# Kernel tuning notes

Hardware: AMD Instinct MI355X
Metric: run time of the kernel (lower is better)

## Reference

```python
import jax, jax.numpy as jnp
import numpy as np

DIM = 1024
N_HEADS = 16
HEAD_DIM = DIM // N_HEADS
MAX_CTX = 2048


def build_rope_cache(seq_len, head_dim, base=10000.0):
    inv_freq = 1.0 / (base ** (jnp.arange(0, head_dim, 2, dtype=jnp.float32) / head_dim))
    t = jnp.arange(seq_len, dtype=jnp.float32)
    freqs = jnp.einsum('i,j->ij', t, inv_freq)  # [T, head_dim//2]
    return jnp.cos(freqs), jnp.sin(freqs)


def apply_rope(x, cos, sin):
    # x: [B, H, T, D]; interleaved even/odd rotation
    x1 = x[..., 0::2]
    x2 = x[..., 1::2]
    c = cos[None, None, :x.shape[-2], :]
    s = sin[None, None, :x.shape[-2], :]
    rx1 = x1 * c - x2 * s
    rx2 = x1 * s + x2 * c
    return jnp.stack([rx1, rx2], axis=-1).reshape(x.shape)


def setup_inputs() -> dict:
    key = jax.random.key(0)
    k1, k2, k3 = jax.random.split(key, 3)
    B, T = 2, 2048
    x = jax.random.normal(k1, (B, T, DIM), dtype=jnp.float32)
    # torch nn.Linear weight shapes: [out_features, in_features]
    qkv_w = jax.random.normal(k2, (3 * DIM, DIM), dtype=jnp.float32) * (1.0 / np.sqrt(DIM))
    out_w = jax.random.normal(k3, (DIM, DIM), dtype=jnp.float32) * (1.0 / np.sqrt(DIM))
    return {"x": x, "qkv_w": qkv_w, "out_w": out_w}


def reference(x, qkv_w, out_w):
    B, T, C = x.shape
    cos, sin = build_rope_cache(MAX_CTX, HEAD_DIM)
    cos = cos.astype(x.dtype)
    sin = sin.astype(x.dtype)

    qkv = jnp.einsum('btc,dc->btd', x, qkv_w)  # [B, T, 3C]
    qkv = qkv.reshape(B, T, 3, N_HEADS, HEAD_DIM).transpose(2, 0, 3, 1, 4)
    q, k, v = qkv[0], qkv[1], qkv[2]  # each [B, H, T, D]

    q = apply_rope(q, cos, sin)
    k = apply_rope(k, cos, sin)

    scale = 1.0 / np.sqrt(HEAD_DIM)
    scores = jnp.einsum('bhqd,bhkd->bhqk', q, k) * scale  # [B, H, T, T]
    causal = jnp.tril(jnp.ones((T, T), dtype=bool))
    scores = jnp.where(causal[None, None], scores, jnp.finfo(scores.dtype).min)
    attn = jax.nn.softmax(scores, axis=-1)
    y = jnp.einsum('bhqk,bhkd->bhqd', attn, v)  # [B, H, T, D]
    y = y.transpose(0, 2, 1, 3).reshape(B, T, C)
    return jnp.einsum('btc,dc->btd', y, out_w)
```

## Files before the change

### kernel.cpp

```cpp
#include <hip/hip_runtime.h>
#include <hip/hip_bf16.h>
#include <cstdint>
#include <cstddef>

#define B_SZ   2
#define T_CTX  2048
#define DIM_C  1024
#define NHEAD  16
#define HD     64
#define NBH    (B_SZ*NHEAD)

typedef __attribute__((ext_vector_type(8))) short short8;
typedef __attribute__((ext_vector_type(4))) float f32x4;
typedef __attribute__((ext_vector_type(16))) float f32x16;

union BV8 { short8 s; __hip_bfloat16 h[8]; unsigned short u[8]; };
union U32x4 { uint32_t u[4]; short8 s8; };

#define GLD16(gp, lp) \
  __builtin_amdgcn_global_load_lds((const __attribute__((address_space(1))) void*)(gp), \
                                   (__attribute__((address_space(3))) void*)(lp), 16, 0, 0)

__device__ inline uint32_t pkbf(float a, float b) {
  union { __hip_bfloat16 h; unsigned short u; } ua, ub;
  ua.h = __float2bfloat16(a);
  ub.h = __float2bfloat16(b);
  return ((uint32_t)ub.u << 16) | (uint32_t)ua.u;
}

__global__ __launch_bounds__(256) void cvt_all(const float* __restrict__ x,
                                               const float* __restrict__ wq,
                                               const float* __restrict__ wo,
                                               __hip_bfloat16* __restrict__ xb,
                                               __hip_bfloat16* __restrict__ wqb,
                                               __hip_bfloat16* __restrict__ wob) {
  int i = blockIdx.x * 256 + threadIdx.x;
  const float* src;
  __hip_bfloat16* dst;
  int off;
  if (i < 1048576) { src = x; dst = xb; off = i; }
  else if (i < 1835008) { src = wq; dst = wqb; off = i - 1048576; }
  else { src = wo; dst = wob; off = i - 1835008; }
  float4 v = reinterpret_cast<const float4*>(src)[off];
  BV8 o;
  o.h[0] = __float2bfloat16(v.x);
  o.h[1] = __float2bfloat16(v.y);
  o.h[2] = __float2bfloat16(v.z);
  o.h[3] = __float2bfloat16(v.w);
  ushort4 st = { o.u[0], o.u[1], o.u[2], o.u[3] };
  reinterpret_cast<ushort4*>(dst)[off] = st;
}

template <typename OutT, int BN>
__global__ __launch_bounds__(256) void gemm_bt(const __hip_bfloat16* __restrict__ A,
                                               const __hip_bfloat16* __restrict__ Bt,
                                               OutT* __restrict__ C,
                                               int M, int N, int K) {
  constexpr int NB = BN / 32;
  constexpr int ABYT = 128 * 128;
  constexpr int BBYT = BN * 128;
  __shared__ __align__(16) char smem[2 * (ABYT + BBYT)];
  const int tid = threadIdx.x;
  const int w = tid >> 6, l = tid & 63;
  const int l15 = l & 15, l4 = l >> 4;
  const int wr = w >> 1, wc = w & 1;
  const int gx = (int)gridDim.x;
  const int nwg = gx * (int)gridDim.y;
  int lin = (int)blockIdx.y * gx + (int)blockIdx.x;
  lin = (lin & 7) * (nwg >> 3) + (lin >> 3);
  const long bm = (long)(lin / gx) * 128;
  const long bn = (long)(lin % gx) * BN;

  f32x4 acc[4][NB] = {};

  const int srow = tid >> 3;
  const int scol = (tid & 7) * 16;
  const int ssw  = scol ^ ((srow & 7) << 4);
  const char* Ab  = (const char*)A;
  const char* Btb = (const char*)Bt;

#define GSTAGE(kt_, buf_)                                                                \
  {                                                                                      \
    char* base_ = smem + (buf_) * (ABYT + BBYT);                                         \
    _Pragma("unroll")                                                                    \
    for (int it = 0; it < 4; ++it) {                                                     \
      long arow = bm + it * 32 + srow;                                                   \
      GLD16(Ab + (arow * K + (kt_)) * 2 + ssw, base_ + it * 4096 + w * 1024);            \
    }                                                                                    \
    _Pragma("unroll")                                                                    \
    for (int it = 0; it < BN / 32; ++it) {                                               \
      long brow = bn + it * 32 + srow;                                                   \
      GLD16(Btb + (brow * K + (kt_)) * 2 + ssw, base_ + ABYT + it * 4096 + w * 1024);    \
    }                                                                                    \
  }

  GSTAGE(0, 0)

  int cur = 0;
  for (int kt = 0; kt < K; kt += 64) {
    __syncthreads();
    if (kt + 64 < K) GSTAGE(kt + 64, cur ^ 1)
    const char* Ac = smem + cur * (ABYT + BBYT);
    const char* Bc = Ac + ABYT;
#pragma unroll
    for (int ksub = 0; ksub < 2; ++ksub) {
      short8 aF[4], bF[NB];
#pragma unroll
      for (int m = 0; m < 4; ++m) {
        int R = wr * 64 + m * 16 + l15;
        aF[m] = *(const short8*)(Ac + R * 128 + ((ksub * 64 + l4 * 16) ^ ((R & 7) << 4)));
      }
#pragma unroll
      for (int n = 0; n < NB; ++n) {
        int R = wc * (BN / 2) + n * 16 + l15;
        bF[n] = *(const short8*)(Bc + R * 128 + ((ksub * 64 + l4 * 16) ^ ((R & 7) << 4)));
      }
#pragma unroll
      for (int m = 0; m < 4; ++m)
#pragma unroll
        for (int n = 0; n < NB; ++n)
          acc[m][n] = __builtin_amdgcn_mfma_f32_16x16x32_bf16(aF[m], bF[n], acc[m][n], 0, 0, 0);
    }
    cur ^= 1;
  }
#undef GSTAGE

#pragma unroll
  for (int m = 0; m < 4; ++m)
#pragma unroll
    for (int n = 0; n < NB; ++n)
#pragma unroll
      for (int r = 0; r < 4; ++r) {
        long row = bm + wr * 64 + m * 16 + l4 * 4 + r;
        long col = bn + wc * (BN / 2) + n * 16 + l15;
        float v = acc[m][n][r];
        if constexpr (sizeof(OutT) == 2) {
          C[row * N + col] = __float2bfloat16(v);
        } else {
          C[row * N + col] = v;
        }
      }
}

__global__ __launch_bounds__(256) void rope_pack(const __hip_bfloat16* __restrict__ qkv,
                                                 __hip_bfloat16* __restrict__ Qb,
                                                 __hip_bfloat16* __restrict__ Kb,
                                                 __hip_bfloat16* __restrict__ VTb) {
  __shared__ __hip_bfloat16 vt[64][72];
  const int bh = blockIdx.x;
  const int b = bh >> 4, h = bh & 15;
  const int t0 = blockIdx.y * 64;
  const int tid = threadIdx.x;
  const float QSCL = 0.125f * 1.4426950408889634f;

#pragma unroll
  for (int rep = 0; rep < 2; ++rep) {
    int idx = rep * 256 + tid;
    int tt = idx >> 3;
    int d0 = (idx & 7) * 8;
    int t = t0 + tt;
    size_t src = ((size_t)(b * T_CTX + t)) * 3072 + h * 64 + d0;
    BV8 qv, kv, vv, qo, ko;
    qv.s = *(const short8*)(qkv + src);
    kv.s = *(const short8*)(qkv + src + 1024);
    vv.s = *(const short8*)(qkv + src + 2048);
#pragma unroll
    for (int p = 0; p < 4; ++p) {
      int i = (d0 >> 1) + p;
      float inv = exp2f(-13.287712379549449f * ((float)(2 * i) * (1.0f / 64.0f)));
      float ang = (float)t * inv;
      float sn, cn;
      sincosf(ang, &sn, &cn);
      float q1 = __bfloat162float(qv.h[2 * p]);
      float q2 = __bfloat162float(qv.h[2 * p + 1]);
      float k1 = __bfloat162float(kv.h[2 * p]);
      float k2 = __bfloat162float(kv.h[2 * p + 1]);
      qo.h[2 * p]     = __float2bfloat16((q1 * cn - q2 * sn) * QSCL);
      qo.h[2 * p + 1] = __float2bfloat16((q1 * sn + q2 * cn) * QSCL);
      ko.h[2 * p]     = __float2bfloat16(k1 * cn - k2 * sn);
      ko.h[2 * p + 1] = __float2bfloat16(k1 * sn + k2 * cn);
    }
    size_t dst = ((size_t)bh * T_CTX + t) * 64 + d0;
    *(short8*)(Qb + dst) = qo.s;
    *(short8*)(Kb + dst) = ko.s;
#pragma unroll
    for (int j = 0; j < 8; ++j) vt[d0 + j][tt] = vv.h[j];
  }
  __syncthreads();
#pragma unroll
  for (int rep = 0; rep < 2; ++rep) {
    int idx = rep * 256 + tid;
    int d = idx >> 3;
    int toff = (idx & 7) * 8;
    BV8 o;
#pragma unroll
    for (int j = 0; j < 8; ++j) o.h[j] = vt[d][toff + j];
    *(short8*)(VTb + ((size_t)bh * 64 + d) * T_CTX + t0 + toff) = o.s;
  }
}

__global__ __launch_bounds__(512) void flash_attn(const __hip_bfloat16* __restrict__ Qb,
                                                  const __hip_bfloat16* __restrict__ Kb,
                                                  const __hip_bfloat16* __restrict__ VTb,
                                                  __hip_bfloat16* __restrict__ Y) {
  __shared__ __align__(16) char smem[67584];
  const int bh = blockIdx.x;
  const int b = bh >> 4, h = bh & 15;
  const int y = blockIdx.y;
  const int jA = 15 - y;
  const int jB = y;
  const int tmaxA = 2 * jA + 1;
  const int tmaxB = 2 * jB + 1;
  const int tid = threadIdx.x;
  const int w = tid >> 6, l = tid & 63;
  const int qsub = w >> 1, kh = w & 1;
  const int l31 = l & 31, hh = l >> 5;
  const int sw7 = (l31 & 7) << 4;
  const int rowb = w * 8 + (l >> 3);
  const int colS = (l & 7) * 16;

#define STAGE1(gg)                                                                     \
  {                                                                                    \
    const int tt_ = ((gg) <= tmaxA) ? (gg) : (gg) - tmaxA - 1;                         \
    const int kv0_ = tt_ << 6;                                                         \
    char* base_ = smem + (((gg) >> 1) & 1) * 32768 + ((gg) & 1) * 16384;               \
    int sw = colS ^ ((rowb & 7) << 4);                                                 \
    GLD16((const char*)Kb + (((size_t)bh * T_CTX + kv0_ + rowb) << 7) + sw,            \
          base_ + w * 1024);                                                           \
    GLD16((const char*)VTb + ((((size_t)bh * 64 + rowb) * T_CTX + kv0_) << 1) + sw,    \
          base_ + 8192 + w * 1024);                                                    \
  }

  f32x16 oA0 = {}, oA1 = {}, oB0 = {}, oB1 = {};
  float lrA = 0.0f, lrB = 0.0f;

  STAGE1(0)
  STAGE1(1)

  int rr = 0;
#pragma unroll
  for (int ph = 0; ph < 2; ++ph) {
    const int slab = ph ? jB : jA;
    const int tmax = ph ? tmaxB : tmaxA;
    const int Q0 = slab * 128 + qsub * 32;
    const int qglob = Q0 + l31;
    f32x16& od0 = ph ? oB0 : oA0;
    f32x16& od1 = ph ? oB1 : oA1;
    float& lrw = ph ? lrB : lrA;

    short8 qB[4];
#pragma unroll
    for (int dblk = 0; dblk < 4; ++dblk)
      qB[dblk] = *(const short8*)(Qb + ((size_t)bh * T_CTX + qglob) * 64 + dblk * 16 + hh * 8);

    for (int t = 0; t <= tmax; ++t, ++rr) {
      if ((rr & 1) == 0) {
        __syncthreads();
        if (rr + 2 <= 33) STAGE1(rr + 2)
        if (rr + 3 <= 33) STAGE1(rr + 3)
      }
      const char* KsB = smem + ((rr >> 1) & 1) * 32768 + (rr & 1) * 16384;
      const char* VsB = KsB + 8192;
      const int kv0 = t << 6;
      const int kbase0 = kv0 + kh * 32;

      if (kbase0 <= Q0 + 31) {
        short8 kA[4];
#pragma unroll
        for (int dblk = 0; dblk < 4; ++dblk)
          kA[dblk] = *(const short8*)(KsB + (kh * 32 + l31) * 128 + ((dblk * 32 + hh * 16) ^ sw7));
        short8 vA[2][2];
#pragma unroll
        for (int dt = 0; dt < 2; ++dt)
#pragma unroll
          for (int ks = 0; ks < 2; ++ks)
            vA[dt][ks] = *(const short8*)(VsB + (dt * 32 + l31) * 128 +
                                          ((kh * 64 + ks * 32 + hh * 16) ^ sw7));

        f32x16 sT = {};
#pragma unroll
        for (int dblk = 0; dblk < 4; ++dblk) {
          __builtin_amdgcn_s_setprio(1);
          sT = __builtin_amdgcn_mfma_f32_32x32x16_bf16(kA[dblk], qB[dblk], sT, 0, 0, 0);
          __builtin_amdgcn_s_setprio(0);
        }
        if (kbase0 + 31 > Q0) {
          const int kbase = kbase0 + 4 * hh;
#pragma unroll
          for (int r = 0; r < 16; ++r) {
            int kg = kbase + (r & 3) + 8 * (r >> 2);
            sT[r] = (kg > qglob) ? -1e30f : sT[r];
          }
        }
        float s8[8];
#pragma unroll
        for (int i = 0; i < 8; ++i) {
          sT[i]     = __builtin_amdgcn_exp2f(sT[i]);
          sT[i + 8] = __builtin_amdgcn_exp2f(sT[i + 8]);
          s8[i] = sT[i] + sT[i + 8];
        }
        lrw += ((s8[0] + s8[1]) + (s8[2] + s8[3])) + ((s8[4] + s8[5]) + (s8[6] + s8[7]));
        uint32_t wk[8];
#pragma unroll
        for (int i = 0; i < 8; ++i) wk[i] = pkbf(sT[2 * i], sT[2 * i + 1]);
#pragma unroll
        for (int ks = 0; ks < 2; ++ks) {
          const int base = ks * 4;
          uint32_t own0 = wk[base + 0], own1 = wk[base + 1];
          uint32_t own2 = wk[base + 2], own3 = wk[base + 3];
          uint32_t e0 = (uint32_t)__shfl_xor((int)(hh ? own0 : own2), 32);
          uint32_t e1 = (uint32_t)__shfl_xor((int)(hh ? own1 : own3), 32);
          U32x4 u;
          u.u[0] = hh ? e0 : own0;
          u.u[1] = hh ? e1 : own1;
          u.u[2] = hh ? own2 : e0;
          u.u[3] = hh ? own3 : e1;
          __builtin_amdgcn_s_setprio(1);
          od0 = __builtin_amdgcn_mfma_f32_32x32x16_bf16(vA[0][ks], u.s8, od0, 0, 0, 0);
          od1 = __builtin_amdgcn_mfma_f32_32x32x16_bf16(vA[1][ks], u.s8, od1, 0, 0, 0);
          __builtin_amdgcn_s_setprio(0);
        }
      }
    }
  }

  lrA += __shfl_xor(lrA, 32);
  lrB += __shfl_xor(lrB, 32);

  __syncthreads();
  {
    float* exch = (float*)smem;
    float* lst = exch + 16384;
    const int slotA = (0 * 4 + qsub) * 2 + kh;
    const int slotB = (1 * 4 + qsub) * 2 + kh;
    const f32x16& nA = kh ? oA0 : oA1;
    const f32x16& nB = kh ? oB0 : oB1;
#pragma unroll
    for (int m = 0; m < 4; ++m) {
      int c = ((2 * m + hh) ^ (l31 & 7)) * 4;
      f32x4 va, vb;
#pragma unroll
      for (int i = 0; i < 4; ++i) { va[i] = nA[m * 4 + i]; vb[i] = nB[m * 4 + i]; }
      *(f32x4*)(exch + slotA * 1024 + l31 * 32 + c) = va;
      *(f32x4*)(exch + slotB * 1024 + l31 * 32 + c) = vb;
    }
    if (hh == 0) {
      lst[slotA * 32 + l31] = lrA;
      lst[slotB * 32 + l31] = lrB;
    }
    __syncthreads();
    const int pA = (0 * 4 + qsub) * 2 + (kh ^ 1);
    const int pB = (1 * 4 + qsub) * 2 + (kh ^ 1);
    float ltA = lrA + lst[pA * 32 + l31];
    float ltB = lrB + lst[pB * 32 + l31];
    f32x16& ownA = kh ? oA1 : oA0;
    f32x16& ownB = kh ? oB1 : oB0;
#pragma unroll
    for (int m = 0; m < 4; ++m) {
      int c = ((2 * m + hh) ^ (l31 & 7)) * 4;
      f32x4 aA = *(const f32x4*)(exch + pA * 1024 + l31 * 32 + c);
      f32x4 aB = *(const f32x4*)(exch + pB * 1024 + l31 * 32 + c);
#pragma unroll
      for (int i = 0; i < 4; ++i) { ownA[m * 4 + i] += aA[i]; ownB[m * 4 + i] += aB[i]; }
    }
#pragma unroll
    for (int sl = 0; sl < 2; ++sl) {
      const f32x16& ov = sl ? ownB : ownA;
      float inv = 1.0f / (sl ? ltB : ltA);
      int q0s = (sl ? jB : jA) * 128 + qsub * 32;
      size_t rowoff = ((size_t)(b * T_CTX + q0s + l31)) * DIM_C + h * 64 + kh * 32;
#pragma unroll
      for (int m = 0; m < 4; ++m) {
        union { ushort4 v; unsigned short us[4]; } st;
#pragma unroll
        for (int i = 0; i < 4; ++i) {
          union { __hip_bfloat16 h2; unsigned short u; } cv;
          cv.h2 = __float2bfloat16(ov[m * 4 + i] * inv);
          st.us[i] = cv.u;
        }
        *(ushort4*)(Y + rowoff + 8 * m + 4 * hh) = st.v;
      }
    }
  }
#undef STAGE1
}

extern "C" void kernel_launch(void* const* d_in, const int* in_sizes, int n_in,
                              void* d_out, int out_size, void* d_ws, size_t ws_size,
                              hipStream_t stream) {
  const float* x     = (const float*)d_in[0];
  const float* qkv_w = (const float*)d_in[1];
  const float* out_w = (const float*)d_in[2];
  float* out = (float*)d_out;

  char* ws = (char*)d_ws;
  const size_t MB = 1024 * 1024;
  __hip_bfloat16* xb    = (__hip_bfloat16*)(ws + 0 * MB);
  __hip_bfloat16* wqkvb = (__hip_bfloat16*)(ws + 8 * MB);
  __hip_bfloat16* woutb = (__hip_bfloat16*)(ws + 14 * MB);
  __hip_bfloat16* qkvb  = (__hip_bfloat16*)(ws + 16 * MB);
  __hip_bfloat16* Qb    = (__hip_bfloat16*)(ws + 40 * MB);
  __hip_bfloat16* Kb    = (__hip_bfloat16*)(ws + 48 * MB);
  __hip_bfloat16* VTb   = (__hip_bfloat16*)(ws + 56 * MB);
  __hip_bfloat16* yb    = (__hip_bfloat16*)(ws + 64 * MB);

  cvt_all<<<8192, 256, 0, stream>>>(x, qkv_w, out_w, xb, wqkvb, woutb);

  gemm_bt<__hip_bfloat16, 192><<<dim3(16, 32), 256, 0, stream>>>(xb, wqkvb, qkvb, 4096, 3072, 1024);

  rope_pack<<<dim3(32, 32), 256, 0, stream>>>(qkvb, Qb, Kb, VTb);

  flash_attn<<<dim3(NBH, 8), 512, 0, stream>>>(Qb, Kb, VTb, yb);

  gemm_bt<float, 64><<<dim3(16, 32), 256, 0, stream>>>(yb, woutb, out, 4096, 1024, 1024);
}
```

Before: 96.48 us.

## Add dedicated QKV GEMM kernel with 128x384 tiles and 8 waves

Replaces the generic 128x192-tile QKV projection GEMM with a specialized kernel that uses 512 threads and a 128x384 output tile, giving 256 workgroups instead of 512. Each wave computes a 64x96 sub-tile, so each A fragment is reused across more B columns and the A matrix is loaded from global memory fewer times. The cost is higher LDS use (about 128KB double-buffered), more accumulator registers per thread and fewer workgroups, which could lower occupancy and cause load imbalance across the 256 CUs.

```diff
diff --git a/kernel.cpp b/kernel.cpp
--- a/kernel.cpp
+++ b/kernel.cpp
@@ -51,6 +51,88 @@
   reinterpret_cast<ushort4*>(dst)[off] = st;
 }
 
+__global__ __launch_bounds__(512) void gemm_qkv(const __hip_bfloat16* __restrict__ A,
+                                                const __hip_bfloat16* __restrict__ Bt,
+                                                __hip_bfloat16* __restrict__ C) {
+  constexpr int K = 1024, N = 3072;
+  constexpr int ABYT = 128 * 128;
+  constexpr int BBYT = 384 * 128;
+  __shared__ __align__(16) char smem[2 * (ABYT + BBYT)];
+  const int tid = threadIdx.x;
+  const int w = tid >> 6, l = tid & 63;
+  const int l15 = l & 15, l4 = l >> 4;
+  const int wr = w >> 2, wc = w & 3;
+  int lin = (int)blockIdx.y * 8 + (int)blockIdx.x;
+  lin = (lin & 7) * 32 + (lin >> 3);
+  const long bm = (long)(lin >> 3) * 128;
+  const long bn = (long)(lin & 7) * 384;
+
+  f32x4 acc[4][6] = {};
+
+  const int srow = tid >> 3;
+  const int scol = (tid & 7) * 16;
+  const int ssw  = scol ^ ((srow & 7) << 4);
+  const char* Ab  = (const char*)A;
+  const char* Btb = (const char*)Bt;
+
+#define GSTAGE(kt_, buf_)                                                                \
+  {                                                                                      \
+    char* base_ = smem + (buf_) * (ABYT + BBYT);                                         \
+    _Pragma("unroll")                                                                    \
+    for (int it = 0; it < 2; ++it) {                                                     \
+      long arow = bm + it * 64 + srow;                                                   \
+      GLD16(Ab + (arow * K + (kt_)) * 2 + ssw, base_ + it * 8192 + w * 1024);            \
+    }                                                                                    \
+    _Pragma("unroll")                                                                    \
+    for (int it = 0; it < 6; ++it) {                                                     \
+      long brow = bn + it * 64 + srow;                                                   \
+      GLD16(Btb + (brow * K + (kt_)) * 2 + ssw, base_ + ABYT + it * 8192 + w * 1024);    \
+    }                                                                                    \
+  }
+
+  GSTAGE(0, 0)
+
+  int cur = 0;
+  for (int kt = 0; kt < K; kt += 64) {
+    __syncthreads();
+    if (kt + 64 < K) GSTAGE(kt + 64, cur ^ 1)
+    const char* Ac = smem + cur * (ABYT + BBYT);
+    const char* Bc = Ac + ABYT;
+#pragma unroll
+    for (int ksub = 0; ksub < 2; ++ksub) {
+      short8 aF[4], bF[6];
+#pragma unroll
+      for (int m = 0; m < 4; ++m) {
+        int R = wr * 64 + m * 16 + l15;
+        aF[m] = *(const short8*)(Ac + R * 128 + ((ksub * 64 + l4 * 16) ^ ((R & 7) << 4)));
+      }
+#pragma unroll
+      for (int n = 0; n < 6; ++n) {
+        int R = wc * 96 + n * 16 + l15;
+        bF[n] = *(const short8*)(Bc + R * 128 + ((ksub * 64 + l4 * 16) ^ ((R & 7) << 4)));
+      }
+#pragma unroll
+      for (int m = 0; m < 4; ++m)
+#pragma unroll
+        for (int n = 0; n < 6; ++n)
+          acc[m][n] = __builtin_amdgcn_mfma_f32_16x16x32_bf16(aF[m], bF[n], acc[m][n], 0, 0, 0);
+    }
+    cur ^= 1;
+  }
+#undef GSTAGE
+
+#pragma unroll
+  for (int m = 0; m < 4; ++m)
+#pragma unroll
+    for (int n = 0; n < 6; ++n)
+#pragma unroll
+      for (int r = 0; r < 4; ++r) {
+        long row = bm + wr * 64 + m * 16 + l4 * 4 + r;
+        long col = bn + wc * 96 + n * 16 + l15;
+        C[row * N + col] = __float2bfloat16(acc[m][n][r]);
+      }
+}
+
 template <typename OutT, int BN>
 __global__ __launch_bounds__(256) void gemm_bt(const __hip_bfloat16* __restrict__ A,
                                                const __hip_bfloat16* __restrict__ Bt,
@@ -406,7 +488,7 @@
 
   cvt_all<<<8192, 256, 0, stream>>>(x, qkv_w, out_w, xb, wqkvb, woutb);
 
-  gemm_bt<__hip_bfloat16, 192><<<dim3(16, 32), 256, 0, stream>>>(xb, wqkvb, qkvb, 4096, 3072, 1024);
+  gemm_qkv<<<dim3(8, 32), 512, 0, stream>>>(xb, wqkvb, qkvb);
 
   rope_pack<<<dim3(32, 32), 256, 0, stream>>>(qkvb, Qb, Kb, VTb);
 
```

After: 97.16 us. Within noise of the previous version (+0.7%).
